# Kernel tuning notes

Hardware: AMD Instinct MI355X
Metric: run time of the kernel (lower is better)

## Reference

```python
import jax, jax.numpy as jnp
import numpy as np

K_NEAREST = 10

def setup_inputs() -> dict:
    key = jax.random.key(0)
    k0, k1, k2, k3 = jax.random.split(key, 4)
    B, D, C = 2048, 128, 100000  # batch, state_dim, memory capacity
    state = jax.random.normal(k0, (B, D), dtype=jnp.float32)
    scale = 1.0 / np.sqrt(D)
    W1 = jax.random.normal(k1, (D, D), dtype=jnp.float32) * scale
    b1 = jnp.zeros((D,), dtype=jnp.float32)
    W2 = jax.random.normal(k2, (D, D), dtype=jnp.float32) * scale
    b2 = jnp.zeros((D,), dtype=jnp.float32)
    memory = jax.random.normal(k3, (C, D), dtype=jnp.float32)
    return {"state": state, "W1": W1, "b1": b1, "W2": W2, "b2": b2, "memory": memory}

def reference(state, W1, b1, W2, b2, memory):
    # encoder: Linear -> ReLU -> Linear
    h = jax.nn.relu(state @ W1 + b1)
    enc = h @ W2 + b2                                  # [B, D]
    sq = (jnp.sum(enc * enc, axis=-1, keepdims=True)
          + jnp.sum(memory * memory, axis=-1)[None, :]
          - 2.0 * (enc @ memory.T))                    # [B, C]
    dist = jnp.sqrt(jnp.maximum(sq, 1e-12))
    # k smallest distances -> mean
    neg_topk, _ = jax.lax.top_k(-dist, K_NEAREST)      # [B, k]
    novelty = jnp.mean(-neg_topk, axis=-1)             # [B]
    return novelty
```

## Files before the change

kernel.cpp:

```cpp
#include <hip/hip_runtime.h>

typedef unsigned short u16;
typedef __bf16 bf16x8 __attribute__((ext_vector_type(8)));
typedef float f32x4 __attribute__((ext_vector_type(4)));

#define DEV __device__ __forceinline__
#define MED3 __builtin_amdgcn_fmed3f
#define MFMA __builtin_amdgcn_mfma_f32_16x16x32_bf16

constexpr int D       = 128;
constexpr int NB      = 2048;
constexpr int C_REAL  = 100000;
constexpr int BN      = 128;
constexpr int NSPLIT  = 32;
constexpr int CHUNKS  = 25;
constexpr int CPAD    = NSPLIT * CHUNKS * BN;
constexpr int BM      = 256;

constexpr size_t OFF_MEMB = 0;
constexpr size_t OFF_MEMN = (size_t)CPAD * D * 2;
constexpr size_t OFF_ENCB = OFF_MEMN + (size_t)CPAD * 4;
constexpr size_t OFF_ENCN = OFF_ENCB + (size_t)NB * D * 2;
constexpr size_t OFF_PART = OFF_ENCN + (size_t)NB * 4;

DEV u16 f2bf(float x) {
    unsigned u = __float_as_uint(x);
    u += 0x7FFFu + ((u >> 16) & 1u);
    return (u16)(u >> 16);
}
DEV float bf2f(u16 b) { return __uint_as_float(((unsigned)b) << 16); }

struct L10 { float a,b,c,d,e,f,g,h,i,j; };

DEV void linit(L10& L) {
    L.a=L.b=L.c=L.d=L.e=L.f=L.g=L.h=L.i=L.j = __builtin_inff();
}
DEV void ins(L10& L, float x) {
    L.j = MED3(L.i, L.j, x);
    L.i = MED3(L.h, L.i, x);
    L.h = MED3(L.g, L.h, x);
    L.g = MED3(L.f, L.g, x);
    L.f = MED3(L.e, L.f, x);
    L.e = MED3(L.d, L.e, x);
    L.d = MED3(L.c, L.d, x);
    L.c = MED3(L.b, L.c, x);
    L.b = MED3(L.a, L.b, x);
    L.a = fminf(L.a, x);
}
DEV void mergeX(L10& L, int d) {
    float ta=__shfl_xor(L.a,d), tb=__shfl_xor(L.b,d), tc=__shfl_xor(L.c,d);
    float td=__shfl_xor(L.d,d), te=__shfl_xor(L.e,d), tf=__shfl_xor(L.f,d);
    float tg=__shfl_xor(L.g,d), th=__shfl_xor(L.h,d), ti=__shfl_xor(L.i,d);
    float tj=__shfl_xor(L.j,d);
    ins(L,ta); ins(L,tb); ins(L,tc); ins(L,td); ins(L,te);
    ins(L,tf); ins(L,tg); ins(L,th); ins(L,ti); ins(L,tj);
}
DEV void storeL(const L10& L, float* dst) {
    dst[0]=L.a; dst[1]=L.b; dst[2]=L.c; dst[3]=L.d; dst[4]=L.e;
    dst[5]=L.f; dst[6]=L.g; dst[7]=L.h; dst[8]=L.i; dst[9]=L.j;
}

__global__ __launch_bounds__(128)
void k_encoder(const float* __restrict__ state, const float* __restrict__ W1,
               const float* __restrict__ b1, const float* __restrict__ W2,
               const float* __restrict__ b2, u16* __restrict__ encB,
               float* __restrict__ encN)
{
    __shared__ __align__(16) float sA[8][128];
    __shared__ __align__(16) float sH[8][128];
    const int tid = threadIdx.x;
    const int rbase = blockIdx.x * 8;

#pragma unroll
    for (int r = 0; r < 8; ++r)
        sA[r][tid] = state[(size_t)(rbase + r) * D + tid];
    __syncthreads();

    float acc[8];
#pragma unroll
    for (int r = 0; r < 8; ++r) acc[r] = b1[tid];
    for (int d4 = 0; d4 < 32; ++d4) {
        float w0 = W1[(d4 * 4 + 0) * D + tid];
        float w1 = W1[(d4 * 4 + 1) * D + tid];
        float w2 = W1[(d4 * 4 + 2) * D + tid];
        float w3 = W1[(d4 * 4 + 3) * D + tid];
#pragma unroll
        for (int r = 0; r < 8; ++r) {
            float4 sv = *reinterpret_cast<const float4*>(&sA[r][d4 * 4]);
            acc[r] = fmaf(sv.w, w3, fmaf(sv.z, w2, fmaf(sv.y, w1, fmaf(sv.x, w0, acc[r]))));
        }
    }
#pragma unroll
    for (int r = 0; r < 8; ++r) sH[r][tid] = fmaxf(acc[r], 0.f);
    __syncthreads();

#pragma unroll
    for (int r = 0; r < 8; ++r) acc[r] = b2[tid];
    for (int d4 = 0; d4 < 32; ++d4) {
        float w0 = W2[(d4 * 4 + 0) * D + tid];
        float w1 = W2[(d4 * 4 + 1) * D + tid];
        float w2 = W2[(d4 * 4 + 2) * D + tid];
        float w3 = W2[(d4 * 4 + 3) * D + tid];
#pragma unroll
        for (int r = 0; r < 8; ++r) {
            float4 sv = *reinterpret_cast<const float4*>(&sH[r][d4 * 4]);
            acc[r] = fmaf(sv.w, w3, fmaf(sv.z, w2, fmaf(sv.y, w1, fmaf(sv.x, w0, acc[r]))));
        }
    }

#pragma unroll
    for (int r = 0; r < 8; ++r) {
        u16 bb = f2bf(acc[r]);
        encB[(size_t)(rbase + r) * D + tid] = bb;
        float vv = bf2f(bb);
        sA[r][tid] = vv * vv;
    }
    __syncthreads();
    if (tid < 8) {
        float s = 0.f;
        for (int d = 0; d < 128; ++d) s += sA[tid][d];
        encN[rbase + tid] = s;
    }
}

__global__ __launch_bounds__(256)
void k_memprep(const float* __restrict__ mem, u16* __restrict__ memB,
               float* __restrict__ memN)
{
    int g = blockIdx.x * 256 + threadIdx.x;
    int row = g >> 5;
    int l32 = g & 31;
    if (row >= CPAD) return;
    float4 v = make_float4(0.f, 0.f, 0.f, 0.f);
    bool real = row < C_REAL;
    if (real)
        v = *reinterpret_cast<const float4*>(mem + (size_t)row * D + l32 * 4);
    u16 c0 = f2bf(v.x), c1 = f2bf(v.y), c2 = f2bf(v.z), c3 = f2bf(v.w);
    float r0 = bf2f(c0), r1 = bf2f(c1), r2 = bf2f(c2), r3 = bf2f(c3);
    uint2 pk;
    pk.x = (unsigned)c0 | ((unsigned)c1 << 16);
    pk.y = (unsigned)c2 | ((unsigned)c3 << 16);
    *reinterpret_cast<uint2*>(memB + (size_t)row * D + l32 * 4) = pk;
    float s = r0 * r0 + r1 * r1 + r2 * r2 + r3 * r3;
    s += __shfl_xor(s, 16);
    s += __shfl_xor(s, 8);
    s += __shfl_xor(s, 4);
    s += __shfl_xor(s, 2);
    s += __shfl_xor(s, 1);
    if (l32 == 0) memN[row] = real ? s : __builtin_inff();
}

__global__ __launch_bounds__(512)
__attribute__((amdgpu_waves_per_eu(2, 2)))
void k_dist(const u16* __restrict__ encB,
            const u16* __restrict__ memB, const float* __restrict__ memN,
            float* __restrict__ partials)
{
    __shared__ __align__(16) unsigned char btile[2][32768];

    const int tid = threadIdx.x;
    const int w   = tid >> 6;
    const int l   = tid & 63;
    const int l15 = l & 15;
    const int lg  = l >> 4;
    const int split = blockIdx.x;
    const int rbase = blockIdx.y * BM;
    const long cbase0 = (long)split * (CHUNKS * BN);

    const u16* ap0 = encB + (size_t)(rbase + w * 32 + l15) * D;
    const u16* ap1 = encB + (size_t)(rbase + w * 32 + 16 + l15) * D;
    bf16x8 a00 = *reinterpret_cast<const bf16x8*>(ap0 + 0 * 32 + lg * 8);
    bf16x8 a01 = *reinterpret_cast<const bf16x8*>(ap0 + 1 * 32 + lg * 8);
    bf16x8 a02 = *reinterpret_cast<const bf16x8*>(ap0 + 2 * 32 + lg * 8);
    bf16x8 a03 = *reinterpret_cast<const bf16x8*>(ap0 + 3 * 32 + lg * 8);
    bf16x8 a10 = *reinterpret_cast<const bf16x8*>(ap1 + 0 * 32 + lg * 8);
    bf16x8 a11 = *reinterpret_cast<const bf16x8*>(ap1 + 1 * 32 + lg * 8);
    bf16x8 a12 = *reinterpret_cast<const bf16x8*>(ap1 + 2 * 32 + lg * 8);
    bf16x8 a13 = *reinterpret_cast<const bf16x8*>(ap1 + 3 * 32 + lg * 8);

    L10 T0,T1,T2,T3,T4,T5,T6,T7;
    linit(T0); linit(T1); linit(T2); linit(T3);
    linit(T4); linit(T5); linit(T6); linit(T7);

    int wsrcoff[4];
#pragma unroll
    for (int u = 0; u < 4; ++u) {
        int p = (u << 13) | (tid << 4);
        wsrcoff[u] = p ^ (((p >> 8) & 7) << 4);
    }
    const int rbl = ((l15 << 8) | (lg << 4)) ^ ((l15 & 7) << 4);
    const int off0 = rbl ^ (0 << 6);
    const int off1 = rbl ^ (1 << 6);
    const int off2 = rbl ^ (2 << 6);
    const int off3 = rbl ^ (3 << 6);

    uint4 s0, s1, s2, s3;
    {
        const unsigned char* src = (const unsigned char*)(memB + cbase0 * D);
        s0 = *reinterpret_cast<const uint4*>(src + wsrcoff[0]);
        s1 = *reinterpret_cast<const uint4*>(src + wsrcoff[1]);
        s2 = *reinterpret_cast<const uint4*>(src + wsrcoff[2]);
        s3 = *reinterpret_cast<const uint4*>(src + wsrcoff[3]);
    }

#define KEY8(A0, A1, MN) do { \
    ins(T0, fmaf(-2.0f, (A0)[0], (MN))); \
    ins(T1, fmaf(-2.0f, (A0)[1], (MN))); \
    ins(T2, fmaf(-2.0f, (A0)[2], (MN))); \
    ins(T3, fmaf(-2.0f, (A0)[3], (MN))); \
    ins(T4, fmaf(-2.0f, (A1)[0], (MN))); \
    ins(T5, fmaf(-2.0f, (A1)[1], (MN))); \
    ins(T6, fmaf(-2.0f, (A1)[2], (MN))); \
    ins(T7, fmaf(-2.0f, (A1)[3], (MN))); \
} while (0)

#define DO_CG(CGI, MNV) do { \
    bf16x8 q0 = *reinterpret_cast<const bf16x8*>(bp + (off0 + ((CGI) << 12))); \
    bf16x8 q1 = *reinterpret_cast<const bf16x8*>(bp + (off1 + ((CGI) << 12))); \
    bf16x8 q2 = *reinterpret_cast<const bf16x8*>(bp + (off2 + ((CGI) << 12))); \
    bf16x8 q3 = *reinterpret_cast<const bf16x8*>(bp + (off3 + ((CGI) << 12))); \
    f32x4 ac0 = {0.f, 0.f, 0.f, 0.f}; \
    f32x4 ac1 = {0.f, 0.f, 0.f, 0.f}; \
    ac0 = MFMA(a00, q0, ac0, 0, 0, 0); \
    ac1 = MFMA(a10, q0, ac1, 0, 0, 0); \
    ac0 = MFMA(a01, q1, ac0, 0, 0, 0); \
    ac1 = MFMA(a11, q1, ac1, 0, 0, 0); \
    ac0 = MFMA(a02, q2, ac0, 0, 0, 0); \
    ac1 = MFMA(a12, q2, ac1, 0, 0, 0); \
    ac0 = MFMA(a03, q3, ac0, 0, 0, 0); \
    ac1 = MFMA(a13, q3, ac1, 0, 0, 0); \
    KEY8(ac0, ac1, (MNV)); \
} while (0)

#pragma unroll 1
    for (int ch = 0; ch < CHUNKS; ++ch) {
        unsigned char* wb = &btile[ch & 1][0];
        *reinterpret_cast<uint4*>(wb + ((0 << 13) | (tid << 4))) = s0;
        *reinterpret_cast<uint4*>(wb + ((1 << 13) | (tid << 4))) = s1;
        *reinterpret_cast<uint4*>(wb + ((2 << 13) | (tid << 4))) = s2;
        *reinterpret_cast<uint4*>(wb + ((3 << 13) | (tid << 4))) = s3;
        {
            int chn = (ch + 1 < CHUNKS) ? ch + 1 : ch;
            const unsigned char* src =
                (const unsigned char*)(memB + (cbase0 + (long)chn * BN) * D);
            s0 = *reinterpret_cast<const uint4*>(src + wsrcoff[0]);
            s1 = *reinterpret_cast<const uint4*>(src + wsrcoff[1]);
            s2 = *reinterpret_cast<const uint4*>(src + wsrcoff[2]);
            s3 = *reinterpret_cast<const uint4*>(src + wsrcoff[3]);
        }
        __syncthreads();

        const long cbase = cbase0 + (long)ch * BN;
        const float* mnp = memN + cbase + l15;
        float mn0 = mnp[0 * 16], mn1 = mnp[1 * 16], mn2 = mnp[2 * 16], mn3 = mnp[3 * 16];
        float mn4 = mnp[4 * 16], mn5 = mnp[5 * 16], mn6 = mnp[6 * 16], mn7 = mnp[7 * 16];

        const unsigned char* bp = &btile[ch & 1][0];
        DO_CG(0, mn0);
        DO_CG(1, mn1);
        DO_CG(2, mn2);
        DO_CG(3, mn3);
        DO_CG(4, mn4);
        DO_CG(5, mn5);
        DO_CG(6, mn6);
        DO_CG(7, mn7);
    }

#define MERGE_STORE(T, LI) do { \
    mergeX(T, 1); mergeX(T, 2); mergeX(T, 4); mergeX(T, 8); \
    if (l15 == 0) { \
        int row = rbase + w * 32 + ((LI) >> 2) * 16 + lg * 4 + ((LI) & 3); \
        storeL(T, partials + (size_t)row * (NSPLIT * 10) + split * 10); \
    } \
} while (0)

    MERGE_STORE(T0, 0);
    MERGE_STORE(T1, 1);
    MERGE_STORE(T2, 2);
    MERGE_STORE(T3, 3);
    MERGE_STORE(T4, 4);
    MERGE_STORE(T5, 5);
    MERGE_STORE(T6, 6);
    MERGE_STORE(T7, 7);
}

__global__ __launch_bounds__(256)
void k_final(const float* __restrict__ partials, const float* __restrict__ encN,
             float* __restrict__ out)
{
    const int w = threadIdx.x >> 6;
    const int l = threadIdx.x & 63;
    const int row = blockIdx.x * 4 + w;

    L10 L;
    linit(L);
    const float* p = partials + (size_t)row * (NSPLIT * 10) + l * 5;
    ins(L, p[0]); ins(L, p[1]); ins(L, p[2]); ins(L, p[3]); ins(L, p[4]);
    mergeX(L, 1); mergeX(L, 2); mergeX(L, 4);
    mergeX(L, 8); mergeX(L, 16); mergeX(L, 32);
    if (l == 0) {
        float en = encN[row];
        float s = 0.f;
        s += sqrtf(fmaxf(en + L.a, 1e-12f));
        s += sqrtf(fmaxf(en + L.b, 1e-12f));
        s += sqrtf(fmaxf(en + L.c, 1e-12f));
        s += sqrtf(fmaxf(en + L.d, 1e-12f));
        s += sqrtf(fmaxf(en + L.e, 1e-12f));
        s += sqrtf(fmaxf(en + L.f, 1e-12f));
        s += sqrtf(fmaxf(en + L.g, 1e-12f));
        s += sqrtf(fmaxf(en + L.h, 1e-12f));
        s += sqrtf(fmaxf(en + L.i, 1e-12f));
        s += sqrtf(fmaxf(en + L.j, 1e-12f));
        out[row] = s * 0.1f;
    }
}

extern "C" void kernel_launch(void* const* d_in, const int* in_sizes, int n_in,
                              void* d_out, int out_size, void* d_ws, size_t ws_size,
                              hipStream_t stream)
{
    const float* state = (const float*)d_in[0];
    const float* W1    = (const float*)d_in[1];
    const float* b1    = (const float*)d_in[2];
    const float* W2    = (const float*)d_in[3];
    const float* b2    = (const float*)d_in[4];
    const float* mem   = (const float*)d_in[5];
    float* out = (float*)d_out;
    char* ws = (char*)d_ws;
    u16*   memB = (u16*)(ws + OFF_MEMB);
    float* memN = (float*)(ws + OFF_MEMN);
    u16*   encB = (u16*)(ws + OFF_ENCB);
    float* encN = (float*)(ws + OFF_ENCN);
    float* partials = (float*)(ws + OFF_PART);

    hipLaunchKernelGGL(k_encoder, dim3(NB / 8), dim3(128), 0, stream,
                       state, W1, b1, W2, b2, encB, encN);
    hipLaunchKernelGGL(k_memprep, dim3(CPAD * 32 / 256), dim3(256), 0, stream,
                       mem, memB, memN);
    hipLaunchKernelGGL(k_dist, dim3(NSPLIT, NB / BM), dim3(512), 0, stream,
                       encB, memB, memN, partials);
    hipLaunchKernelGGL(k_final, dim3(NB / 4), dim3(256), 0, stream,
                       partials, encN, out);
}
```

Baseline: 235.3 us.

## Stage memory tiles via global_load_lds, guard top-k inserts, use min-merge at end

```diff
diff --git a/kernel.cpp b/kernel.cpp
--- a/kernel.cpp
+++ b/kernel.cpp
@@ -47,6 +47,9 @@
     L.b = MED3(L.a, L.b, x);
     L.a = fminf(L.a, x);
 }
+DEV void insg(L10& L, float x) {
+    if (x < L.j) ins(L, x);
+}
 DEV void mergeX(L10& L, int d) {
     float ta=__shfl_xor(L.a,d), tb=__shfl_xor(L.b,d), tc=__shfl_xor(L.c,d);
     float td=__shfl_xor(L.d,d), te=__shfl_xor(L.e,d), tf=__shfl_xor(L.f,d);
@@ -54,6 +57,15 @@
     float tj=__shfl_xor(L.j,d);
     ins(L,ta); ins(L,tb); ins(L,tc); ins(L,td); ins(L,te);
     ins(L,tf); ins(L,tg); ins(L,th); ins(L,ti); ins(L,tj);
+}
+DEV void mergeMin(L10& L, int d) {
+    float ra=__shfl_xor(L.a,d), rb=__shfl_xor(L.b,d), rc=__shfl_xor(L.c,d);
+    float rd_=__shfl_xor(L.d,d), re=__shfl_xor(L.e,d), rf=__shfl_xor(L.f,d);
+    float rg=__shfl_xor(L.g,d), rh=__shfl_xor(L.h,d), ri=__shfl_xor(L.i,d);
+    float rj=__shfl_xor(L.j,d);
+    L.a=fminf(L.a,rj); L.b=fminf(L.b,ri); L.c=fminf(L.c,rh); L.d=fminf(L.d,rg);
+    L.e=fminf(L.e,rf); L.f=fminf(L.f,re); L.g=fminf(L.g,rd_); L.h=fminf(L.h,rc);
+    L.i=fminf(L.i,rb); L.j=fminf(L.j,ra);
 }
 DEV void storeL(const L10& L, float* dst) {
     dst[0]=L.a; dst[1]=L.b; dst[2]=L.c; dst[3]=L.d; dst[4]=L.e;
@@ -194,24 +206,33 @@
     const int off2 = rbl ^ (2 << 6);
     const int off3 = rbl ^ (3 << 6);
 
-    uint4 s0, s1, s2, s3;
-    {
-        const unsigned char* src = (const unsigned char*)(memB + cbase0 * D);
-        s0 = *reinterpret_cast<const uint4*>(src + wsrcoff[0]);
-        s1 = *reinterpret_cast<const uint4*>(src + wsrcoff[1]);
-        s2 = *reinterpret_cast<const uint4*>(src + wsrcoff[2]);
-        s3 = *reinterpret_cast<const uint4*>(src + wsrcoff[3]);
-    }
+#define STAGE(B, CH) do { \
+    const unsigned char* sb_ = (const unsigned char*)(memB + (cbase0 + (long)(CH) * BN) * D); \
+    __builtin_amdgcn_global_load_lds( \
+        (const __attribute__((address_space(1))) unsigned char*)(sb_ + wsrcoff[0]), \
+        (__attribute__((address_space(3))) unsigned char*)(&btile[0][0] + (((B) << 15) | (0 << 13) | (w << 10))), 16, 0, 0); \
+    __builtin_amdgcn_global_load_lds( \
+        (const __attribute__((address_space(1))) unsigned char*)(sb_ + wsrcoff[1]), \
+        (__attribute__((address_space(3))) unsigned char*)(&btile[0][0] + (((B) << 15) | (1 << 13) | (w << 10))), 16, 0, 0); \
+    __builtin_amdgcn_global_load_lds( \
+        (const __attribute__((address_space(1))) unsigned char*)(sb_ + wsrcoff[2]), \
+        (__attribute__((address_space(3))) unsigned char*)(&btile[0][0] + (((B) << 15) | (2 << 13) | (w << 10))), 16, 0, 0); \
+    __builtin_amdgcn_global_load_lds( \
+        (const __attribute__((address_space(1))) unsigned char*)(sb_ + wsrcoff[3]), \
+        (__attribute__((address_space(3))) unsigned char*)(&btile[0][0] + (((B) << 15) | (3 << 13) | (w << 10))), 16, 0, 0); \
+} while (0)
 
 #define KEY8(A0, A1, MN) do { \
-    ins(T0, fmaf(-2.0f, (A0)[0], (MN))); \
-    ins(T1, fmaf(-2.0f, (A0)[1], (MN))); \
-    ins(T2, fmaf(-2.0f, (A0)[2], (MN))); \
-    ins(T3, fmaf(-2.0f, (A0)[3], (MN))); \
-    ins(T4, fmaf(-2.0f, (A1)[0], (MN))); \
-    ins(T5, fmaf(-2.0f, (A1)[1], (MN))); \
-    ins(T6, fmaf(-2.0f, (A1)[2], (MN))); \
-    ins(T7, fmaf(-2.0f, (A1)[3], (MN))); \
+    float k0_ = fmaf(-2.0f, (A0)[0], (MN)); \
+    float k1_ = fmaf(-2.0f, (A0)[1], (MN)); \
+    float k2_ = fmaf(-2.0f, (A0)[2], (MN)); \
+    float k3_ = fmaf(-2.0f, (A0)[3], (MN)); \
+    float k4_ = fmaf(-2.0f, (A1)[0], (MN)); \
+    float k5_ = fmaf(-2.0f, (A1)[1], (MN)); \
+    float k6_ = fmaf(-2.0f, (A1)[2], (MN)); \
+    float k7_ = fmaf(-2.0f, (A1)[3], (MN)); \
+    insg(T0, k0_); insg(T1, k1_); insg(T2, k2_); insg(T3, k3_); \
+    insg(T4, k4_); insg(T5, k5_); insg(T6, k6_); insg(T7, k7_); \
 } while (0)
 
 #define DO_CG(CGI, MNV) do { \
@@ -232,23 +253,12 @@
     KEY8(ac0, ac1, (MNV)); \
 } while (0)
 
+    STAGE(0, 0);
+    __syncthreads();
+
 #pragma unroll 1
     for (int ch = 0; ch < CHUNKS; ++ch) {
-        unsigned char* wb = &btile[ch & 1][0];
-        *reinterpret_cast<uint4*>(wb + ((0 << 13) | (tid << 4))) = s0;
-        *reinterpret_cast<uint4*>(wb + ((1 << 13) | (tid << 4))) = s1;
-        *reinterpret_cast<uint4*>(wb + ((2 << 13) | (tid << 4))) = s2;
-        *reinterpret_cast<uint4*>(wb + ((3 << 13) | (tid << 4))) = s3;
-        {
-            int chn = (ch + 1 < CHUNKS) ? ch + 1 : ch;
-            const unsigned char* src =
-                (const unsigned char*)(memB + (cbase0 + (long)chn * BN) * D);
-            s0 = *reinterpret_cast<const uint4*>(src + wsrcoff[0]);
-            s1 = *reinterpret_cast<const uint4*>(src + wsrcoff[1]);
-            s2 = *reinterpret_cast<const uint4*>(src + wsrcoff[2]);
-            s3 = *reinterpret_cast<const uint4*>(src + wsrcoff[3]);
-        }
-        __syncthreads();
+        if (ch + 1 < CHUNKS) STAGE((ch + 1) & 1, ch + 1);
 
         const long cbase = cbase0 + (long)ch * BN;
         const float* mnp = memN + cbase + l15;
@@ -264,10 +274,11 @@
         DO_CG(5, mn5);
         DO_CG(6, mn6);
         DO_CG(7, mn7);
+        __syncthreads();
     }
 
 #define MERGE_STORE(T, LI) do { \
-    mergeX(T, 1); mergeX(T, 2); mergeX(T, 4); mergeX(T, 8); \
+    mergeX(T, 1); mergeX(T, 2); mergeX(T, 4); mergeMin(T, 8); \
     if (l15 == 0) { \
         int row = rbase + w * 32 + ((LI) >> 2) * 16 + lg * 4 + ((LI) & 3); \
         storeL(T, partials + (size_t)row * (NSPLIT * 10) + split * 10); \
@@ -297,7 +308,7 @@
     const float* p = partials + (size_t)row * (NSPLIT * 10) + l * 5;
     ins(L, p[0]); ins(L, p[1]); ins(L, p[2]); ins(L, p[3]); ins(L, p[4]);
     mergeX(L, 1); mergeX(L, 2); mergeX(L, 4);
-    mergeX(L, 8); mergeX(L, 16); mergeX(L, 32);
+    mergeX(L, 8); mergeX(L, 16); mergeMin(L, 32);
     if (l == 0) {
         float en = encN[row];
         float s = 0.f;
```

New measurement: 262.1 us. 11.4% more time.
